# Kernel tuning notes

Measured on AMD Instinct MI355X. Metric: run time of the kernel, lower is better.

## Reference

```python
import jax, jax.numpy as jnp
import numpy as np

F_THRESHOLD = 10  # zero out DCT coefficients with i + j <= 10 (low-frequency triangle)


def _dct_mat(N):
    # torch_dct.dct with norm=None: X_k = 2 * sum_n x_n cos(pi*(2n+1)*k/(2N))
    n = np.arange(N)
    k = np.arange(N)[:, None]
    return (2.0 * np.cos(np.pi * (2 * n + 1) * k / (2 * N))).astype(np.float32)  # [k, n]


def _idct_mat(N):
    # inverse of the norm=None DCT-II above: x_n = (1/N) * sum_k w_k X_k cos(pi*(2n+1)*k/(2N)), w_0=0.5
    n = np.arange(N)[:, None]
    k = np.arange(N)
    w = np.ones(N, dtype=np.float64)
    w[0] = 0.5
    return ((w * np.cos(np.pi * (2 * n + 1) * k / (2 * N))) / N).astype(np.float32)  # [n, k]


def _filtermask(H, W):
    i = jnp.arange(H)[:, None]
    j = jnp.arange(W)[None, :]
    return jnp.where(i + j <= F_THRESHOLD, 0.0, 1.0).astype(jnp.float32)  # [H, W]


def setup_inputs() -> dict:
    key = jax.random.key(0)
    im = jax.random.normal(key, (32, 3, 512, 512), dtype=jnp.float32)
    return {"im": im}


def reference(im) -> jnp.ndarray:
    B, C, H, W = im.shape
    Ch = jnp.asarray(_dct_mat(H))   # [kh, h]
    Cw = jnp.asarray(_dct_mat(W))   # [kw, w]
    Dh = jnp.asarray(_idct_mat(H))  # [h, kh]
    Dw = jnp.asarray(_idct_mat(W))  # [w, kw]
    mask = _filtermask(H, W)

    # dct_2d: DCT-II along W then along H
    x = jnp.einsum('kh,bchw,lw->bckl', Ch, im, Cw)
    x = x * mask  # zero low-frequency triangle
    # idct_2d
    x = jnp.einsum('hk,bckl,wl->bchw', Dh, x, Dw)
    return x
```

## Files before the change

kernel.cpp:

```cpp
#include <hip/hip_runtime.h>
#include <math.h>

#define NPIX 512
#define NK 11
#define NKP 12
#define NPAIR 121
#define RBLKS 8
#define NCH 96

#if __has_builtin(__builtin_amdgcn_cosf)
__device__ inline float cos_rev(float rev) { return __builtin_amdgcn_cosf(rev); }
#else
__device__ inline float cos_rev(float rev) { return __cosf(rev * 6.28318530717958647692f); }
#endif

__device__ inline float ctab(int h, int k) {
    int m = ((2 * h + 1) * k) & 2047;
    return 2.0f * cos_rev((float)m * (1.0f / 2048.0f));
}

#if __has_builtin(__builtin_amdgcn_update_dpp)
template <int CTRL>
__device__ inline float dpp_add(float x) {
    int xi = __builtin_bit_cast(int, x);
    int yi = __builtin_amdgcn_update_dpp(0, xi, CTRL, 0xf, 0xf, false);
    return x + __builtin_bit_cast(float, yi);
}
__device__ inline float red16(float x) {
    x = dpp_add<0x128>(x);
    x = dpp_add<0x124>(x);
    x = dpp_add<0x122>(x);
    x = dpp_add<0x121>(x);
    return x;
}
#else
__device__ inline float red16(float x) {
    x += __shfl_xor(x, 8);
    x += __shfl_xor(x, 4);
    x += __shfl_xor(x, 2);
    x += __shfl_xor(x, 1);
    return x;
}
#endif

__device__ inline void build_Cs64(float (*Cs64)[NKP], int t, int row0) {
#pragma unroll
    for (int j = 0; j < 3; ++j) {
        int idx = j * 256 + t;
        int hl = idx / NKP;
        int kk = idx - hl * NKP;
        Cs64[hl][kk] = (kk < NK) ? ctab(row0 + hl, kk) : 0.f;
    }
}

#define FMA4(ACC, CC) ACC.x += (CC) * v.x; ACC.y += (CC) * v.y; ACC.z += (CC) * v.z; ACC.w += (CC) * v.w;
#define DOT4(ACC) ((ACC).x * cl0 + (ACC).y * cl1 + (ACC).z * cl2 + (ACC).w * cl3)

__global__ __launch_bounds__(256, 4) void k_partial(const float* __restrict__ im,
                                                    float* __restrict__ plow) {
    __shared__ float Cs64[64][NKP];
    __shared__ float red[16][NPAIR];

    int bid = blockIdx.x;
    int c = bid >> 3, rb = bid & 7;
    int t = threadIdx.x;
    int row0 = rb * 64;

    build_Cs64(Cs64, t, row0);
    __syncthreads();

    int half = t >> 7;
    int col4 = t & 127;
    int w0 = col4 * 4;
    int hbase = half * 32;
    const float* imc = im + (size_t)c * NPIX * NPIX + (size_t)(row0 + hbase) * NPIX + w0;

    float4 z = make_float4(0.f, 0.f, 0.f, 0.f);
    float4 a0 = z, a1 = z, a2 = z, a3 = z, a4 = z, a5 = z, a6 = z, a7 = z, a8 = z, a9 = z, a10 = z;

#pragma unroll 4
    for (int i = 0; i < 32; ++i) {
        float4 v = *(const float4*)(imc + (size_t)i * NPIX);
        const float4* crow = (const float4*)&Cs64[hbase + i][0];
        float4 c0 = crow[0], c1 = crow[1], c2 = crow[2];
        FMA4(a0, c0.x) FMA4(a1, c0.y) FMA4(a2, c0.z) FMA4(a3, c0.w)
        FMA4(a4, c1.x) FMA4(a5, c1.y) FMA4(a6, c1.z) FMA4(a7, c1.w)
        FMA4(a8, c2.x) FMA4(a9, c2.y) FMA4(a10, c2.z)
    }

    int g = t >> 4;
    for (int l = 0; l < NK; ++l) {
        float cl0 = ctab(w0 + 0, l);
        float cl1 = ctab(w0 + 1, l);
        float cl2 = ctab(w0 + 2, l);
        float cl3 = ctab(w0 + 3, l);
        float p0 = red16(DOT4(a0));
        float p1 = red16(DOT4(a1));
        float p2 = red16(DOT4(a2));
        float p3 = red16(DOT4(a3));
        float p4 = red16(DOT4(a4));
        float p5 = red16(DOT4(a5));
        float p6 = red16(DOT4(a6));
        float p7 = red16(DOT4(a7));
        float p8 = red16(DOT4(a8));
        float p9 = red16(DOT4(a9));
        float p10 = red16(DOT4(a10));
        if ((t & 15) == 0) {
            red[g][0 * NK + l] = p0;  red[g][1 * NK + l] = p1;  red[g][2 * NK + l] = p2;
            red[g][3 * NK + l] = p3;  red[g][4 * NK + l] = p4;  red[g][5 * NK + l] = p5;
            red[g][6 * NK + l] = p6;  red[g][7 * NK + l] = p7;  red[g][8 * NK + l] = p8;
            red[g][9 * NK + l] = p9;  red[g][10 * NK + l] = p10;
        }
    }
    __syncthreads();

    if (t < NPAIR) {
        float s = 0.f;
#pragma unroll
        for (int gg = 0; gg < 16; ++gg) s += red[gg][t];
        plow[(size_t)bid * NPAIR + t] = s;
    }
}

__global__ __launch_bounds__(256, 4) void k_output(const float* __restrict__ im,
                                                   const float* __restrict__ plow,
                                                   float* __restrict__ out) {
    __shared__ float Cs64[64][NKP];
    __shared__ float Ls[NPAIR];

    int bid = blockIdx.x;
    int c = bid >> 3, rb = bid & 7;
    int t = threadIdx.x;
    int row0 = rb * 64;

    build_Cs64(Cs64, t, row0);

    if (t < NPAIR) {
        int k = t / NK, l = t % NK;
        float s = 0.f;
        const float* pp = plow + (size_t)c * RBLKS * NPAIR + t;
#pragma unroll
        for (int b = 0; b < RBLKS; ++b) s += pp[b * NPAIR];
        float sk = (k == 0 ? 0.5f : 1.0f) * (1.0f / 1024.0f);
        float sl = (l == 0 ? 0.5f : 1.0f) * (1.0f / 1024.0f);
        Ls[t] = (k + l <= 10) ? s * sk * sl : 0.f;
    }
    __syncthreads();

    int half = t >> 7;
    int col4 = t & 127;
    int w0 = col4 * 4;
    int hbase = half * 32;

    float4 z = make_float4(0.f, 0.f, 0.f, 0.f);
    float4 B0 = z, B1 = z, B2 = z, B3 = z, B4 = z, B5 = z, B6 = z, B7 = z, B8 = z, B9 = z, B10 = z;

#define BADD(BK, KI) { float lw = Ls[(KI) * NK + l]; BK.x += lw * cl0; BK.y += lw * cl1; BK.z += lw * cl2; BK.w += lw * cl3; }
    for (int l = 0; l < NK; ++l) {
        float cl0 = ctab(w0 + 0, l);
        float cl1 = ctab(w0 + 1, l);
        float cl2 = ctab(w0 + 2, l);
        float cl3 = ctab(w0 + 3, l);
        BADD(B0, 0) BADD(B1, 1) BADD(B2, 2) BADD(B3, 3) BADD(B4, 4) BADD(B5, 5)
        BADD(B6, 6) BADD(B7, 7) BADD(B8, 8) BADD(B9, 9) BADD(B10, 10)
    }

    const float* imc = im + (size_t)c * NPIX * NPIX + (size_t)(row0 + hbase) * NPIX + w0;
    float* outc = out + (size_t)c * NPIX * NPIX + (size_t)(row0 + hbase) * NPIX + w0;

#define CORR(comp) (c0.x * B0.comp + c0.y * B1.comp + c0.z * B2.comp + c0.w * B3.comp \
                  + c1.x * B4.comp + c1.y * B5.comp + c1.z * B6.comp + c1.w * B7.comp \
                  + c2.x * B8.comp + c2.y * B9.comp + c2.z * B10.comp)

#pragma unroll 4
    for (int i = 0; i < 32; ++i) {
        float4 v = *(const float4*)(imc + (size_t)i * NPIX);
        const float4* crow = (const float4*)&Cs64[hbase + i][0];
        float4 c0 = crow[0], c1 = crow[1], c2 = crow[2];
        float4 o = make_float4(v.x - CORR(x), v.y - CORR(y), v.z - CORR(z), v.w - CORR(w));
        *(float4*)(outc + (size_t)i * NPIX) = o;
    }
}

extern "C" void kernel_launch(void* const* d_in, const int* in_sizes, int n_in,
                              void* d_out, int out_size, void* d_ws, size_t ws_size,
                              hipStream_t stream) {
    const float* im = (const float*)d_in[0];
    float* out = (float*)d_out;
    float* plow = (float*)d_ws;

    k_partial<<<NCH * RBLKS, 256, 0, stream>>>(im, plow);
    k_output<<<NCH * RBLKS, 256, 0, stream>>>(im, plow, out);
}
```

Measured before the change: 69.38 us.

## Halve rows per block, software-pipeline output loads, use nontemporal stores

Splits each channel into 16 row blocks of 32 rows instead of 8 blocks of 64, doubling the grid to 1536 blocks for better occupancy and load balance. The output kernel loop is manually unrolled into a double-buffered load/compute/store schedule so that global loads are issued ahead of the arithmetic. Output writes use nontemporal stores to avoid polluting the cache. The trade-off is twice as many partial sums written to and reduced from the workspace, and the per-block DCT column table and wave reductions are now amortized over fewer rows.

```diff
diff --git a/kernel.cpp b/kernel.cpp
--- a/kernel.cpp
+++ b/kernel.cpp
@@ -5,8 +5,11 @@
 #define NK 11
 #define NKP 12
 #define NPAIR 121
-#define RBLKS 8
+#define RBLKS 16
+#define BROWS 32
 #define NCH 96
+
+typedef float vfloat4 __attribute__((ext_vector_type(4)));
 
 #if __has_builtin(__builtin_amdgcn_cosf)
 __device__ inline float cos_rev(float rev) { return __builtin_amdgcn_cosf(rev); }
@@ -43,13 +46,15 @@
 }
 #endif
 
-__device__ inline void build_Cs64(float (*Cs64)[NKP], int t, int row0) {
-#pragma unroll
-    for (int j = 0; j < 3; ++j) {
-        int idx = j * 256 + t;
-        int hl = idx / NKP;
-        int kk = idx - hl * NKP;
-        Cs64[hl][kk] = (kk < NK) ? ctab(row0 + hl, kk) : 0.f;
+__device__ inline void build_Cs32(float (*Cs)[NKP], int t, int row0) {
+    {
+        int hl = t / NKP, kk = t - hl * NKP;
+        Cs[hl][kk] = (kk < NK) ? ctab(row0 + hl, kk) : 0.f;
+    }
+    int idx = 256 + t;
+    if (idx < BROWS * NKP) {
+        int hl = idx / NKP, kk = idx - hl * NKP;
+        Cs[hl][kk] = (kk < NK) ? ctab(row0 + hl, kk) : 0.f;
     }
 }
 
@@ -58,30 +63,30 @@
 
 __global__ __launch_bounds__(256, 4) void k_partial(const float* __restrict__ im,
                                                     float* __restrict__ plow) {
-    __shared__ float Cs64[64][NKP];
+    __shared__ float Cs[BROWS][NKP];
     __shared__ float red[16][NPAIR];
 
     int bid = blockIdx.x;
-    int c = bid >> 3, rb = bid & 7;
+    int c = bid >> 4, rb = bid & 15;
     int t = threadIdx.x;
-    int row0 = rb * 64;
-
-    build_Cs64(Cs64, t, row0);
+    int row0 = rb * BROWS;
+
+    build_Cs32(Cs, t, row0);
     __syncthreads();
 
     int half = t >> 7;
     int col4 = t & 127;
     int w0 = col4 * 4;
-    int hbase = half * 32;
+    int hbase = half * 16;
     const float* imc = im + (size_t)c * NPIX * NPIX + (size_t)(row0 + hbase) * NPIX + w0;
 
     float4 z = make_float4(0.f, 0.f, 0.f, 0.f);
     float4 a0 = z, a1 = z, a2 = z, a3 = z, a4 = z, a5 = z, a6 = z, a7 = z, a8 = z, a9 = z, a10 = z;
 
 #pragma unroll 4
-    for (int i = 0; i < 32; ++i) {
+    for (int i = 0; i < 16; ++i) {
         float4 v = *(const float4*)(imc + (size_t)i * NPIX);
-        const float4* crow = (const float4*)&Cs64[hbase + i][0];
+        const float4* crow = (const float4*)&Cs[hbase + i][0];
         float4 c0 = crow[0], c1 = crow[1], c2 = crow[2];
         FMA4(a0, c0.x) FMA4(a1, c0.y) FMA4(a2, c0.z) FMA4(a3, c0.w)
         FMA4(a4, c1.x) FMA4(a5, c1.y) FMA4(a6, c1.z) FMA4(a7, c1.w)
@@ -125,15 +130,15 @@
 __global__ __launch_bounds__(256, 4) void k_output(const float* __restrict__ im,
                                                    const float* __restrict__ plow,
                                                    float* __restrict__ out) {
-    __shared__ float Cs64[64][NKP];
+    __shared__ float Cs[BROWS][NKP];
     __shared__ float Ls[NPAIR];
 
     int bid = blockIdx.x;
-    int c = bid >> 3, rb = bid & 7;
+    int c = bid >> 4, rb = bid & 15;
     int t = threadIdx.x;
-    int row0 = rb * 64;
-
-    build_Cs64(Cs64, t, row0);
+    int row0 = rb * BROWS;
+
+    build_Cs32(Cs, t, row0);
 
     if (t < NPAIR) {
         int k = t / NK, l = t % NK;
@@ -150,7 +155,7 @@
     int half = t >> 7;
     int col4 = t & 127;
     int w0 = col4 * 4;
-    int hbase = half * 32;
+    int hbase = half * 16;
 
     float4 z = make_float4(0.f, 0.f, 0.f, 0.f);
     float4 B0 = z, B1 = z, B2 = z, B3 = z, B4 = z, B5 = z, B6 = z, B7 = z, B8 = z, B9 = z, B10 = z;
@@ -172,14 +177,24 @@
                   + c1.x * B4.comp + c1.y * B5.comp + c1.z * B6.comp + c1.w * B7.comp \
                   + c2.x * B8.comp + c2.y * B9.comp + c2.z * B10.comp)
 
-#pragma unroll 4
-    for (int i = 0; i < 32; ++i) {
-        float4 v = *(const float4*)(imc + (size_t)i * NPIX);
-        const float4* crow = (const float4*)&Cs64[hbase + i][0];
-        float4 c0 = crow[0], c1 = crow[1], c2 = crow[2];
-        float4 o = make_float4(v.x - CORR(x), v.y - CORR(y), v.z - CORR(z), v.w - CORR(w));
-        *(float4*)(outc + (size_t)i * NPIX) = o;
-    }
+#define LOADROW(DST, I) DST = *(const float4*)(imc + (size_t)(I) * NPIX);
+#define STOREROW(SRC, I) { \
+    const float4* crow = (const float4*)&Cs[hbase + (I)][0]; \
+    float4 c0 = crow[0], c1 = crow[1], c2 = crow[2]; \
+    vfloat4 o; \
+    o.x = SRC.x - CORR(x); o.y = SRC.y - CORR(y); \
+    o.z = SRC.z - CORR(z); o.w = SRC.w - CORR(w); \
+    __builtin_nontemporal_store(o, (vfloat4*)(outc + (size_t)(I) * NPIX)); }
+
+    float4 u0, u1, u2, u3, q0, q1, q2, q3;
+    LOADROW(u0, 0)  LOADROW(u1, 1)  LOADROW(u2, 2)  LOADROW(u3, 3)
+    LOADROW(q0, 4)  LOADROW(q1, 5)  LOADROW(q2, 6)  LOADROW(q3, 7)
+    STOREROW(u0, 0)  STOREROW(u1, 1)  STOREROW(u2, 2)  STOREROW(u3, 3)
+    LOADROW(u0, 8)  LOADROW(u1, 9)  LOADROW(u2, 10) LOADROW(u3, 11)
+    STOREROW(q0, 4)  STOREROW(q1, 5)  STOREROW(q2, 6)  STOREROW(q3, 7)
+    LOADROW(q0, 12) LOADROW(q1, 13) LOADROW(q2, 14) LOADROW(q3, 15)
+    STOREROW(u0, 8)  STOREROW(u1, 9)  STOREROW(u2, 10) STOREROW(u3, 11)
+    STOREROW(q0, 12) STOREROW(q1, 13) STOREROW(q2, 14) STOREROW(q3, 15)
 }
 
 extern "C" void kernel_launch(void* const* d_in, const int* in_sizes, int n_in,
```

Result: faster. 67.99 us (-2.0%).
